# Performance work log

Measured on AMD Instinct MI355X. Metric: run time of the kernel, lower is better.

## Reference

```python
import jax, jax.numpy as jnp
import numpy as np

NUM_EXPERTS = 64
TOP_K = 2
NOISE_EPS = 0.01


def setup_inputs() -> dict:
    key = jax.random.key(0)
    k1, k2, k3, k4 = jax.random.split(key, 4)
    B, D, E = 32768, 2048, NUM_EXPERTS
    x = jax.random.normal(k1, (B, D), dtype=jnp.float32)
    # original inits these to zero; use small random weights for a non-degenerate top-k
    w_gate = jax.random.normal(k2, (D, E), dtype=jnp.float32) * 0.02
    w_noise = jax.random.normal(k3, (D, E), dtype=jnp.float32) * 0.02
    noise = jax.random.normal(k4, (B, E), dtype=jnp.float32)  # tf.random.normal draw, fixed
    return {"x": x, "w_gate": w_gate, "w_noise": w_noise, "noise": noise}


def reference(x, w_gate, w_noise, noise):
    # routing_pooling='flatten' on a 2D input is identity
    pooled = x  # [B, D]
    routing = pooled @ w_gate  # [B, E]
    # noisy routing (training=True path)
    noise_stddev = jax.nn.softplus(pooled @ w_noise) + NOISE_EPS
    routing = routing + noise * noise_stddev
    # softmax_top_k: take top k+1, keep top k, softmax, scatter back to E experts
    kk = min(TOP_K + 1, NUM_EXPERTS)
    top_vals, top_idx = jax.lax.top_k(routing, kk)
    top_k_vals = top_vals[:, :TOP_K]            # [B, k]
    top_k_idx = top_idx[:, :TOP_K]              # [B, k]
    top_k_gates = jax.nn.softmax(top_k_vals, axis=-1)
    B = routing.shape[0]
    rows = jnp.arange(B)[:, None]
    # rowwise_unsorted_segment_sum -> scatter gates into expert slots
    out = jnp.zeros((B, NUM_EXPERTS), dtype=routing.dtype).at[rows, top_k_idx].add(top_k_gates)
    return out
```

## Files before the change

### kernel.cpp

```cpp
#include <hip/hip_runtime.h>
#include <math.h>


typedef _Float16 half4v __attribute__((ext_vector_type(4)));
typedef _Float16 half8v __attribute__((ext_vector_type(8)));
typedef float f32x4 __attribute__((ext_vector_type(4)));

constexpr int DIMK = 2048;
constexpr int NEXP = 64;
constexpr int BM   = 64;
constexpr int NCH  = DIMK / 32;

__device__ __forceinline__ void async_load16(const void* g, void* l) {
    __builtin_amdgcn_global_load_lds(
        (const __attribute__((address_space(1))) unsigned int*)g,
        (__attribute__((address_space(3))) unsigned int*)l, 16, 0, 0);
}

__device__ __forceinline__ bool gt_pair(float a, int ia, float b, int ib) {
    return (a > b) || (a == b && ia < ib);
}

__global__ __launch_bounds__(256)
void presplit_kernel(const float* __restrict__ wg, const float* __restrict__ wn,
                     _Float16* __restrict__ wsB)
{
    int gid  = blockIdx.x * 256 + threadIdx.x;
    int lane = gid & 63;
    int t    = (gid >> 6) & 7;
    int c    = gid >> 9;
    int n    = t * 16 + (lane & 15);
    int kb   = c * 32 + ((lane >> 4) << 3);
    const float* src = (n < NEXP) ? (wg + n) : (wn + (n - NEXP));
    half8v h1, h2;
    #pragma unroll
    for (int j = 0; j < 8; ++j) {
        float w = src[(size_t)(kb + j) * NEXP] * 65536.0f;
        _Float16 a = (_Float16)w;
        h1[j] = a;
        h2[j] = (_Float16)(w - (float)a);
    }
    *(half8v*)(wsB + ((((size_t)c * 2 + 0) * 8 + t) * 64 + lane) * 8) = h1;
    *(half8v*)(wsB + ((((size_t)c * 2 + 1) * 8 + t) * 64 + lane) * 8) = h2;
}

__global__ __launch_bounds__(512, 4)
void routing_mfma(const float* __restrict__ x, const _Float16* __restrict__ wsB,
                  const float* __restrict__ noise, float* __restrict__ out)
{
    __shared__ _Float16 Bp[4][2][8][64][8];
    __shared__ float4   cand[BM][2];
    __shared__ float4   res[BM];

    const int tid  = threadIdx.x;
    const int lane = tid & 63;
    const int w    = tid >> 6;
    const int mt   = w >> 1;
    const int wnh  = w & 1;
    const int q    = lane >> 4;
    const int cidx = lane & 15;
    const int row0 = blockIdx.x * BM;

    f32x4  acc[4] = {};
    float4 ra[4][2];

    const float* xr0 = x + (size_t)(row0 + mt * 16 + cidx) * DIMK + q * 8;

    auto issue_B = [&](int c, int buf) {
        #pragma unroll
        for (int ii = 0; ii < 2; ++ii) {
            int idx = w * 2 + ii;
            int p = idx >> 3, t = idx & 7;
            const _Float16* g = wsB + ((((size_t)c * 2 + p) * 8 + t) * 64 + lane) * 8;
            async_load16(g, &Bp[buf][p][t][0][0]);
        }
    };

#define ISSUE_A(C, S)                                            \
    {   const float* pa_ = xr0 + (C) * 32;                       \
        ra[S][0] = *(const float4*)(pa_);                        \
        ra[S][1] = *(const float4*)(pa_ + 4);  }

#define FENCE() asm volatile("" ::: "memory")

#define STEP(C, ISS, WN)                                                     \
    {                                                                        \
        asm volatile("s_waitcnt vmcnt(" #WN ")" ::: "memory");               \
        asm volatile("s_barrier" ::: "memory");                              \
        if (ISS) issue_B((C) + 3, ((C) + 3) & 3);                            \
        half8v af0, af1;                                                     \
        _Pragma("unroll")                                                    \
        for (int h = 0; h < 2; ++h) {                                        \
            float4 v = ra[(C) & 3][h];                                       \
            float f0 = v.x * 1024.f, f1 = v.y * 1024.f;                      \
            float f2 = v.z * 1024.f, f3 = v.w * 1024.f;                      \
            _Float16 a0 = (_Float16)f0, a1 = (_Float16)f1;                   \
            _Float16 a2 = (_Float16)f2, a3 = (_Float16)f3;                   \
            af0[h * 4 + 0] = a0; af0[h * 4 + 1] = a1;                        \
            af0[h * 4 + 2] = a2; af0[h * 4 + 3] = a3;                        \
            af1[h * 4 + 0] = (_Float16)(f0 - (float)a0);                     \
            af1[h * 4 + 1] = (_Float16)(f1 - (float)a1);                     \
            af1[h * 4 + 2] = (_Float16)(f2 - (float)a2);                     \
            af1[h * 4 + 3] = (_Float16)(f3 - (float)a3);                     \
        }                                                                    \
        if (ISS) ISSUE_A((C) + 3, ((C) + 3) & 3);                            \
        __builtin_amdgcn_s_setprio(1);                                       \
        _Pragma("unroll")                                                    \
        for (int tt = 0; tt < 4; ++tt) {                                     \
            int ntile = (tt < 2) ? (wnh * 2 + tt) : (4 + wnh * 2 + (tt - 2));\
            half8v b0 = *(const half8v*)&Bp[(C) & 3][0][ntile][lane][0];     \
            half8v b1 = *(const half8v*)&Bp[(C) & 3][1][ntile][lane][0];     \
            acc[tt] = __builtin_amdgcn_mfma_f32_16x16x32_f16(                \
                af0, b0, acc[tt], 0, 0, 0);                                  \
            acc[tt] = __builtin_amdgcn_mfma_f32_16x16x32_f16(                \
                af0, b1, acc[tt], 0, 0, 0);                                  \
            acc[tt] = __builtin_amdgcn_mfma_f32_16x16x32_f16(                \
                af1, b0, acc[tt], 0, 0, 0);                                  \
        }                                                                    \
        __builtin_amdgcn_s_setprio(0);                                       \
    }

    issue_B(0, 0);
    ISSUE_A(0, 0);
    FENCE();
    issue_B(1, 1);
    ISSUE_A(1, 1);
    FENCE();
    issue_B(2, 2);
    ISSUE_A(2, 2);

    #pragma unroll 1
    for (int cb = 0; cb < NCH - 4; cb += 4) {
        STEP(cb + 0, 1, 8)
        STEP(cb + 1, 1, 8)
        STEP(cb + 2, 1, 8)
        STEP(cb + 3, 1, 8)
    }
    STEP(NCH - 4, 1, 8)
    STEP(NCH - 3, 0, 8)
    STEP(NCH - 2, 0, 4)
    STEP(NCH - 1, 0, 0)

#undef STEP
#undef ISSUE_A
#undef FENCE

    const float s = 0x1p-26f;
    {
        float rv[2][4];
        const int rbase = row0 + mt * 16 + q * 4;
        #pragma unroll
        for (int g = 0; g < 2; ++g) {
            int e = wnh * 32 + g * 16 + cidx;
            #pragma unroll
            for (int r = 0; r < 4; ++r) {
                float nz   = noise[(size_t)(rbase + r) * NEXP + e];
                float gate = acc[g][r] * s;
                float nv   = acc[g + 2][r] * s;
                float sp   = fmaxf(nv, 0.f) + log1pf(expf(-fabsf(nv)));
                rv[g][r]   = gate + nz * (sp + 0.01f);
            }
        }
        #pragma unroll
        for (int r = 0; r < 4; ++r) {
            int e0 = wnh * 32 + cidx, e1 = e0 + 16;
            float v1, v2; int i1, i2;
            float a = rv[0][r], b = rv[1][r];
            if (a >= b) { v1 = a; i1 = e0; v2 = b; i2 = e1; }
            else        { v1 = b; i1 = e1; v2 = a; i2 = e0; }
            #pragma unroll
            for (int m = 1; m <= 8; m <<= 1) {
                float b1 = __shfl_xor(v1, m); int ib1 = __shfl_xor(i1, m);
                float b2 = __shfl_xor(v2, m); int ib2 = __shfl_xor(i2, m);
                if (gt_pair(b1, ib1, v1, i1)) {
                    float o1 = v1; int oi1 = i1;
                    v1 = b1; i1 = ib1;
                    if (gt_pair(b2, ib2, o1, oi1)) { v2 = b2; i2 = ib2; }
                    else                           { v2 = o1; i2 = oi1; }
                } else if (gt_pair(b1, ib1, v2, i2)) {
                    v2 = b1; i2 = ib1;
                }
            }
            if (cidx == 0) {
                int rowb = mt * 16 + q * 4 + r;
                cand[rowb][wnh] = make_float4(v1, __int_as_float(i1),
                                              v2, __int_as_float(i2));
            }
        }
    }
    __syncthreads();

    if (tid < BM) {
        float4 c0 = cand[tid][0], c1 = cand[tid][1];
        float mv1 = c0.x; int mi1 = __float_as_int(c0.y);
        float mv2 = c0.z; int mi2 = __float_as_int(c0.w);
        float b1 = c1.x;  int ib1 = __float_as_int(c1.y);
        float b2 = c1.z;  int ib2 = __float_as_int(c1.w);
        if (gt_pair(b1, ib1, mv1, mi1)) {
            float o1 = mv1; int oi1 = mi1;
            mv1 = b1; mi1 = ib1;
            if (gt_pair(b2, ib2, o1, oi1)) { mv2 = b2; mi2 = ib2; }
            else                           { mv2 = o1; mi2 = oi1; }
        } else if (gt_pair(b1, ib1, mv2, mi2)) {
            mv2 = b1; mi2 = ib1;
        }
        float t  = expf(mv2 - mv1);
        float g1 = 1.f / (1.f + t);
        res[tid] = make_float4(g1, __int_as_float(mi1),
                               t * g1, __int_as_float(mi2));
    }
    __syncthreads();

    {
        int rr  = tid >> 3;
        int seg = tid & 7;
        float4 rv = res[rr];
        float g1 = rv.x, g2 = rv.z;
        int   j1 = __float_as_int(rv.y), j2 = __float_as_int(rv.w);
        float* op = out + (size_t)(row0 + rr) * NEXP + seg * 8;
        #pragma unroll
        for (int qq = 0; qq < 2; ++qq) {
            int e0 = seg * 8 + qq * 4;
            float4 o;
            o.x = (e0 + 0 == j1) ? g1 : ((e0 + 0 == j2) ? g2 : 0.f);
            o.y = (e0 + 1 == j1) ? g1 : ((e0 + 1 == j2) ? g2 : 0.f);
            o.z = (e0 + 2 == j1) ? g1 : ((e0 + 2 == j2) ? g2 : 0.f);
            o.w = (e0 + 3 == j1) ? g1 : ((e0 + 3 == j2) ? g2 : 0.f);
            *(float4*)(op + qq * 4) = o;
        }
    }
}

extern "C" void kernel_launch(void* const* d_in, const int* in_sizes, int n_in,
                              void* d_out, int out_size, void* d_ws, size_t ws_size,
                              hipStream_t stream) {
    const float* x     = (const float*)d_in[0];
    const float* wg    = (const float*)d_in[1];
    const float* wn    = (const float*)d_in[2];
    const float* noise = (const float*)d_in[3];
    float* out = (float*)d_out;
    _Float16* wsB = (_Float16*)d_ws;

    presplit_kernel<<<dim3(128), 256, 0, stream>>>(wg, wn, wsB);

    const int Brows = in_sizes[0] / DIMK;
    dim3 grid(Brows / BM);
    routing_mfma<<<grid, 512, 0, stream>>>(x, wsB, noise, out);
}
```

Baseline: 403.3 us.

## Load B fragments directly from global into registers, dropping LDS staging and barriers

Replaces the 4-stage LDS ring buffer, filled by async global_load_lds with per-step waitcnt and barrier, with per-wave direct global loads of the split-fp16 weight fragments into registers. Loads are double-buffered in registers alongside the x loads. The aim is to remove block-wide barriers and LDS round trips. In exchange each wave loads its own copy of the B tiles, raising L2 traffic, and register pressure rises, which may hurt occupancy at launch_bounds(512,4).

```diff
diff --git a/kernel.cpp b/kernel.cpp
--- a/kernel.cpp
+++ b/kernel.cpp
@@ -10,12 +10,6 @@
 constexpr int NEXP = 64;
 constexpr int BM   = 64;
 constexpr int NCH  = DIMK / 32;
-
-__device__ __forceinline__ void async_load16(const void* g, void* l) {
-    __builtin_amdgcn_global_load_lds(
-        (const __attribute__((address_space(1))) unsigned int*)g,
-        (__attribute__((address_space(3))) unsigned int*)l, 16, 0, 0);
-}
 
 __device__ __forceinline__ bool gt_pair(float a, int ia, float b, int ib) {
     return (a > b) || (a == b && ia < ib);
@@ -48,9 +42,8 @@
 void routing_mfma(const float* __restrict__ x, const _Float16* __restrict__ wsB,
                   const float* __restrict__ noise, float* __restrict__ out)
 {
-    __shared__ _Float16 Bp[4][2][8][64][8];
-    __shared__ float4   cand[BM][2];
-    __shared__ float4   res[BM];
+    __shared__ float4 cand[BM][2];
+    __shared__ float4 res[BM];
 
     const int tid  = threadIdx.x;
     const int lane = tid & 63;
@@ -61,37 +54,34 @@
     const int cidx = lane & 15;
     const int row0 = blockIdx.x * BM;
 
-    f32x4  acc[4] = {};
-    float4 ra[4][2];
-
-    const float* xr0 = x + (size_t)(row0 + mt * 16 + cidx) * DIMK + q * 8;
-
-    auto issue_B = [&](int c, int buf) {
-        #pragma unroll
-        for (int ii = 0; ii < 2; ++ii) {
-            int idx = w * 2 + ii;
-            int p = idx >> 3, t = idx & 7;
-            const _Float16* g = wsB + ((((size_t)c * 2 + p) * 8 + t) * 64 + lane) * 8;
-            async_load16(g, &Bp[buf][p][t][0][0]);
-        }
-    };
-
-#define ISSUE_A(C, S)                                            \
-    {   const float* pa_ = xr0 + (C) * 32;                       \
-        ra[S][0] = *(const float4*)(pa_);                        \
-        ra[S][1] = *(const float4*)(pa_ + 4);  }
-
-#define FENCE() asm volatile("" ::: "memory")
-
-#define STEP(C, ISS, WN)                                                     \
-    {                                                                        \
-        asm volatile("s_waitcnt vmcnt(" #WN ")" ::: "memory");               \
-        asm volatile("s_barrier" ::: "memory");                              \
-        if (ISS) issue_B((C) + 3, ((C) + 3) & 3);                            \
-        half8v af0, af1;                                                     \
+    f32x4 acc[4] = {};
+
+    const float* xp = x + (size_t)(row0 + mt * 16 + cidx) * DIMK + q * 8;
+    const _Float16* bbase = wsB + (size_t)lane * 8;
+
+    half8v bA0[4], bA1[4], bB0[4], bB1[4];
+    float4 rA0, rA1, rB0, rB1;
+
+#define LOADB(C, B0, B1)                                                     \
+    {   const _Float16* p_ = bbase + (size_t)(C) * 8192;                     \
+        _Pragma("unroll")                                                    \
+        for (int tt = 0; tt < 4; ++tt) {                                     \
+            int ntile = (tt < 2) ? (wnh * 2 + tt) : (4 + wnh * 2 + (tt - 2));\
+            B0[tt] = *(const half8v*)(p_ + ntile * 512);                     \
+            B1[tt] = *(const half8v*)(p_ + 4096 + ntile * 512);              \
+        }                                                                    \
+    }
+
+#define LOADX(C, R0, R1)                                                     \
+    {   const float* p_ = xp + (C) * 32;                                     \
+        R0 = *(const float4*)(p_);                                           \
+        R1 = *(const float4*)(p_ + 4);  }
+
+#define COMPUTE(B0, B1, R0, R1)                                              \
+    {   half8v af0, af1;                                                     \
         _Pragma("unroll")                                                    \
         for (int h = 0; h < 2; ++h) {                                        \
-            float4 v = ra[(C) & 3][h];                                       \
+            float4 v = h ? (R1) : (R0);                                      \
             float f0 = v.x * 1024.f, f1 = v.y * 1024.f;                      \
             float f2 = v.z * 1024.f, f3 = v.w * 1024.f;                      \
             _Float16 a0 = (_Float16)f0, a1 = (_Float16)f1;                   \
@@ -103,47 +93,35 @@
             af1[h * 4 + 2] = (_Float16)(f2 - (float)a2);                     \
             af1[h * 4 + 3] = (_Float16)(f3 - (float)a3);                     \
         }                                                                    \
-        if (ISS) ISSUE_A((C) + 3, ((C) + 3) & 3);                            \
-        __builtin_amdgcn_s_setprio(1);                                       \
         _Pragma("unroll")                                                    \
         for (int tt = 0; tt < 4; ++tt) {                                     \
-            int ntile = (tt < 2) ? (wnh * 2 + tt) : (4 + wnh * 2 + (tt - 2));\
-            half8v b0 = *(const half8v*)&Bp[(C) & 3][0][ntile][lane][0];     \
-            half8v b1 = *(const half8v*)&Bp[(C) & 3][1][ntile][lane][0];     \
             acc[tt] = __builtin_amdgcn_mfma_f32_16x16x32_f16(                \
-                af0, b0, acc[tt], 0, 0, 0);                                  \
+                af0, B0[tt], acc[tt], 0, 0, 0);                              \
             acc[tt] = __builtin_amdgcn_mfma_f32_16x16x32_f16(                \
-                af0, b1, acc[tt], 0, 0, 0);                                  \
+                af0, B1[tt], acc[tt], 0, 0, 0);                              \
             acc[tt] = __builtin_amdgcn_mfma_f32_16x16x32_f16(                \
-                af1, b0, acc[tt], 0, 0, 0);                                  \
+                af1, B0[tt], acc[tt], 0, 0, 0);                              \
         }                                                                    \
-        __builtin_amdgcn_s_setprio(0);                                       \
-    }
-
-    issue_B(0, 0);
-    ISSUE_A(0, 0);
-    FENCE();
-    issue_B(1, 1);
-    ISSUE_A(1, 1);
-    FENCE();
-    issue_B(2, 2);
-    ISSUE_A(2, 2);
+    }
+
+    LOADB(0, bA0, bA1);
+    LOADX(0, rA0, rA1);
 
     #pragma unroll 1
-    for (int cb = 0; cb < NCH - 4; cb += 4) {
-        STEP(cb + 0, 1, 8)
-        STEP(cb + 1, 1, 8)
-        STEP(cb + 2, 1, 8)
-        STEP(cb + 3, 1, 8)
-    }
-    STEP(NCH - 4, 1, 8)
-    STEP(NCH - 3, 0, 8)
-    STEP(NCH - 2, 0, 4)
-    STEP(NCH - 1, 0, 0)
-
-#undef STEP
-#undef ISSUE_A
-#undef FENCE
+    for (int c = 0; c < NCH; c += 2) {
+        LOADB(c + 1, bB0, bB1);
+        LOADX(c + 1, rB0, rB1);
+        COMPUTE(bA0, bA1, rA0, rA1);
+        if (c + 2 < NCH) {
+            LOADB(c + 2, bA0, bA1);
+            LOADX(c + 2, rA0, rA1);
+        }
+        COMPUTE(bB0, bB1, rB0, rB1);
+    }
+
+#undef COMPUTE
+#undef LOADX
+#undef LOADB
 
     const float s = 0x1p-26f;
     {
```

After: 485.3 us. +20.3%, slower.
